# Kernel tuning notes

Measured on AMD Instinct MI355X. Metric: run time of the kernel, lower is better.

Reference implementation:

```python
import jax, jax.numpy as jnp
import numpy as np

N_HEADS = 12


def setup_inputs() -> dict:
    key = jax.random.key(0)
    k1, k2, k3 = jax.random.split(key, 3)
    B, W, C = 2, 2048, 768
    in_sequence_bwc = jax.random.normal(k1, (B, W, C), dtype=jnp.float32)
    # QKV projection weight [3C, C] (torch Linear convention: out_features x in_features)
    w_attn = jax.random.normal(k2, (3 * C, C), dtype=jnp.float32) * (1.0 / np.sqrt(C))
    w_proj = jax.random.normal(k3, (C, C), dtype=jnp.float32) * (1.0 / np.sqrt(C))
    return {"in_sequence_bwc": in_sequence_bwc, "w_attn": w_attn, "w_proj": w_proj}


def reference(in_sequence_bwc, w_attn, w_proj):
    B, W, C = in_sequence_bwc.shape
    H = N_HEADS
    K = C // H  # head dim
    qkv = jnp.einsum('bwc,dc->bwd', in_sequence_bwc, w_attn)  # [B,W,3C]
    q, k, v = jnp.split(qkv, 3, axis=-1)
    # [B,H,W,K]
    q = q.reshape(B, W, H, K).transpose(0, 2, 1, 3)
    k = k.reshape(B, W, H, K).transpose(0, 2, 1, 3)
    v = v.reshape(B, W, H, K).transpose(0, 2, 1, 3)
    scores = jnp.einsum('bhqk,bhsk->bhqs', q, k) / jnp.sqrt(jnp.float32(K))
    causal = jnp.tril(jnp.ones((W, W), dtype=bool))
    scores = jnp.where(causal[None, None], scores, jnp.float32(-jnp.inf))
    probs = jax.nn.softmax(scores, axis=-1)
    out = jnp.einsum('bhqs,bhsk->bhqk', probs, v)  # [B,H,W,K]
    out = out.transpose(0, 2, 1, 3).reshape(B, W, C)
    return jnp.einsum('bwc,dc->bwd', out, w_proj)
```

## Files before the change

kernel.cpp:

```cpp
#include <hip/hip_runtime.h>

constexpr int B_  = 2;
constexpr int W_  = 2048;
constexpr int C_  = 768;
constexpr int H_  = 12;
constexpr int HD  = 64;
constexpr int C3  = 3 * C_;
constexpr int M_  = B_ * W_;
constexpr int NSLOT = 80;

typedef float  f32x4 __attribute__((ext_vector_type(4)));
typedef short  s16x8 __attribute__((ext_vector_type(8)));
typedef short  s16x4 __attribute__((ext_vector_type(4)));
typedef unsigned short u16;
typedef unsigned int   u32;

__device__ __forceinline__ u16 f2bf(float f) {
    unsigned int u = __float_as_uint(f);
    u += 0x7FFFu + ((u >> 16) & 1u);
    return (u16)(u >> 16);
}
__device__ __forceinline__ float bf2f(u16 v) {
    return __uint_as_float(((u32)v) << 16);
}

__device__ __forceinline__ void gload_lds16(const u16* g, u16* l) {
    __builtin_amdgcn_global_load_lds(
        (const __attribute__((address_space(1))) unsigned int*)g,
        (__attribute__((address_space(3))) unsigned int*)l, 16, 0, 0);
}

__global__ __launch_bounds__(256)
void cvt_all(const float* __restrict__ x, const float* __restrict__ wa,
             const float* __restrict__ wp, u16* __restrict__ xb,
             u16* __restrict__ wab, u16* __restrict__ wpb)
{
    const int n0 = M_ * C_ / 8;
    const int n1 = n0 + C3 * C_ / 8;
    const int n2 = n1 + C_ * C_ / 8;
    int i = blockIdx.x * 256 + threadIdx.x;
    const float* s; u16* d; int j;
    if (i < n0)      { s = x;  d = xb;  j = i; }
    else if (i < n1) { s = wa; d = wab; j = i - n0; }
    else if (i < n2) { s = wp; d = wpb; j = i - n1; }
    else return;
    const float4 a = reinterpret_cast<const float4*>(s)[j * 2];
    const float4 b = reinterpret_cast<const float4*>(s)[j * 2 + 1];
    s16x8 v;
    v[0] = (short)f2bf(a.x); v[1] = (short)f2bf(a.y);
    v[2] = (short)f2bf(a.z); v[3] = (short)f2bf(a.w);
    v[4] = (short)f2bf(b.x); v[5] = (short)f2bf(b.y);
    v[6] = (short)f2bf(b.z); v[7] = (short)f2bf(b.w);
    reinterpret_cast<s16x8*>(d)[j] = v;
}

__device__ __forceinline__ void store_out(u16*  p, float v) { *p = f2bf(v); }
__device__ __forceinline__ void store_out(float* p, float v) { *p = v; }

template <typename OutT>
__global__ __launch_bounds__(256)
void gemm_nt_mfma(const u16* __restrict__ A, const u16* __restrict__ Bm,
                  OutT* __restrict__ Y, int Ndim, int Kdim)
{
    __shared__ __align__(16) u16 As[3][128 * 32];
    __shared__ __align__(16) u16 Bs[3][128 * 32];

    const int t  = threadIdx.x;
    const int w  = t >> 6;
    const int l  = t & 63;
    const int lg = l >> 4;
    const int ln = l & 15;
    const int wm = w >> 1;
    const int wn = w & 1;
    const int m0 = blockIdx.x * 128;
    const int n0 = blockIdx.y * 128;

    f32x4 acc[4][4];
    #pragma unroll
    for (int mi = 0; mi < 4; ++mi)
        #pragma unroll
        for (int ni = 0; ni < 4; ++ni)
            acc[mi][ni] = (f32x4){0.f, 0.f, 0.f, 0.f};

    size_t off[2];
    #pragma unroll
    for (int it = 0; it < 2; ++it) {
        const int c  = t + it * 256;
        off[it] = (size_t)((c >> 6) * 16 + (c & 15)) * Kdim + ((c >> 4) & 3) * 8;
    }

    #define GEMM_STAGE(buf, k0s)                                              \
        _Pragma("unroll")                                                     \
        for (int it = 0; it < 2; ++it) {                                      \
            gload_lds16(A  + (size_t)m0 * Kdim + (k0s) + off[it],             \
                        &As[buf][(size_t)(it * 256 + w * 64) * 8]);           \
            gload_lds16(Bm + (size_t)n0 * Kdim + (k0s) + off[it],             \
                        &Bs[buf][(size_t)(it * 256 + w * 64) * 8]);           \
        }

    GEMM_STAGE(0, 0)
    GEMM_STAGE(1, 32)

    int cur = 0;
    for (int k0 = 0; k0 < Kdim; k0 += 32) {
        if (k0 + 32 < Kdim)
            asm volatile("s_waitcnt vmcnt(4)" ::: "memory");
        else
            asm volatile("s_waitcnt vmcnt(0)" ::: "memory");
        __builtin_amdgcn_s_barrier();

        const int nx2 = (cur + 2 >= 3) ? cur - 1 : cur + 2;
        if (k0 + 64 < Kdim) { GEMM_STAGE(nx2, k0 + 64) }

        s16x8 af[4], bf[4];
        #pragma unroll
        for (int mi = 0; mi < 4; ++mi)
            af[mi] = *reinterpret_cast<const s16x8*>(
                &As[cur][(size_t)((wm * 4 + mi) * 64 + l) * 8]);
        #pragma unroll
        for (int ni = 0; ni < 4; ++ni)
            bf[ni] = *reinterpret_cast<const s16x8*>(
                &Bs[cur][(size_t)((wn * 4 + ni) * 64 + l) * 8]);
        #pragma unroll
        for (int mi = 0; mi < 4; ++mi)
            #pragma unroll
            for (int ni = 0; ni < 4; ++ni)
                acc[mi][ni] = __builtin_amdgcn_mfma_f32_16x16x32_bf16(
                    af[mi], bf[ni], acc[mi][ni], 0, 0, 0);

        cur = (cur == 2) ? 0 : cur + 1;
    }
    #undef GEMM_STAGE

    #pragma unroll
    for (int mi = 0; mi < 4; ++mi) {
        const int row = m0 + wm * 64 + mi * 16 + lg * 4;
        #pragma unroll
        for (int ni = 0; ni < 4; ++ni) {
            const int col = n0 + wn * 64 + ni * 16 + ln;
            #pragma unroll
            for (int r = 0; r < 4; ++r)
                store_out(&Y[(size_t)(row + r) * Ndim + col], acc[mi][ni][r]);
        }
    }
}

__global__ __launch_bounds__(256)
void attn_partial(const u16* __restrict__ qkv, u16* __restrict__ po,
                  float* __restrict__ pl)
{
    __shared__ __align__(16) unsigned char KsB[64 * 128];
    __shared__ __align__(16) unsigned char VtB[64 * 144];

    const int t  = threadIdx.x;
    const int w  = t >> 6;
    const int l  = t & 63;
    const int lg = l >> 4;
    const int ln = l & 15;
    const int p  = (NSLOT - 1) - (int)blockIdx.x;
    const int h  = blockIdx.y;
    const int b  = blockIdx.z;

    int qt, ck;
    if (p < 8)       { qt = p;                 ck = 0; }
    else if (p < 24) { qt = 8  + ((p - 8) >> 1);  ck = (p - 8) & 1; }
    else if (p < 48) { qt = 16 + (p - 24) / 3;    ck = (p - 24) % 3; }
    else             { qt = 24 + ((p - 48) >> 2); ck = (p - 48) & 3; }

    const int qb  = qt * 64;
    const int q0w = qb + w * 16;
    const int g0  = ck * 8;
    const int g1  = min(qt + 1, g0 + 8);
    const int slot = (b * H_ + h) * NSLOT + p;

    const u16* base  = qkv + (size_t)(b * W_) * C3;
    const u16* kbase = base + C_ + h * HD;
    const u16* vbase = base + 2 * C_ + h * HD;

    s16x8 qf[2];
    {
        const u16* qrow = base + (size_t)(q0w + ln) * C3 + h * HD;
        #pragma unroll
        for (int kc = 0; kc < 2; ++kc)
            qf[kc] = *reinterpret_cast<const s16x8*>(&qrow[kc * 32 + lg * 8]);
    }

    s16x8 onesf;
    {
        const short v1 = (ln == 0) ? (short)0x3F80 : (short)0;
        #pragma unroll
        for (int i = 0; i < 8; ++i) onesf[i] = v1;
    }

    f32x4 o[4];
    #pragma unroll
    for (int i = 0; i < 4; ++i) o[i] = (f32x4){0.f, 0.f, 0.f, 0.f};
    f32x4 o4 = (f32x4){0.f, 0.f, 0.f, 0.f};

    const float c1 = 0.18033688011112042f;
    const float c2 = 17.312340490667562f;

    const size_t sk_off = (size_t)((t >> 7) * 16 + (t & 15)) * C3
                        + ((t >> 6) & 1) * 32 + ((t >> 4) & 3) * 8;
    const bool vstage = (t < 128);
    const int vrun = (t >> 4) & 7;
    const int vK0  = (vrun >> 2) * 32 + (vrun & 3) * 4;
    const int vdq  = (t & 15) * 4;
    const int kfb  = l * 16;

    s16x8 kr[2];
    s16x4 vr[8];

    {
        const int s0 = g0 * 64;
        const u16* ks = kbase + (size_t)s0 * C3 + sk_off;
        kr[0] = *reinterpret_cast<const s16x8*>(ks);
        kr[1] = *reinterpret_cast<const s16x8*>(ks + (size_t)32 * C3);
        if (vstage) {
            const u16* vsrc = vbase + (size_t)(s0 + vK0) * C3 + vdq;
            #pragma unroll
            for (int e = 0; e < 8; ++e)
                vr[e] = *reinterpret_cast<const s16x4*>(
                    &vsrc[(size_t)((e >> 2) * 16 + (e & 3)) * C3]);
        }
    }

    for (int g = g0; g < g1; ++g) {
        const int s0 = g * 64;

        __syncthreads();

        *reinterpret_cast<s16x8*>(KsB + t * 16)         = kr[0];
        *reinterpret_cast<s16x8*>(KsB + (t + 256) * 16) = kr[1];
        if (vstage) {
            #pragma unroll
            for (int j = 0; j < 4; ++j) {
                s16x8 pk = { vr[0][j], vr[1][j], vr[2][j], vr[3][j],
                             vr[4][j], vr[5][j], vr[6][j], vr[7][j] };
                *reinterpret_cast<s16x8*>(
                    VtB + (vdq + j) * 144 + vrun * 16) = pk;
            }
        }

        if (g + 1 < g1) {
            const int s1 = s0 + 64;
            const u16* ks = kbase + (size_t)s1 * C3 + sk_off;
            kr[0] = *reinterpret_cast<const s16x8*>(ks);
            kr[1] = *reinterpret_cast<const s16x8*>(ks + (size_t)32 * C3);
            if (vstage) {
                const u16* vsrc = vbase + (size_t)(s1 + vK0) * C3 + vdq;
                #pragma unroll
                for (int e = 0; e < 8; ++e)
                    vr[e] = *reinterpret_cast<const s16x4*>(
                        &vsrc[(size_t)((e >> 2) * 16 + (e & 3)) * C3]);
            }
        }

        __syncthreads();

        #pragma unroll
        for (int c = 0; c < 2; ++c) {
            if (s0 + c * 32 <= q0w + 15) {
                float pt[2][4];
                #pragma unroll
                for (int n2 = 0; n2 < 2; ++n2) {
                    const unsigned char* kfrag = KsB + (c * 2 + n2) * 2048 + kfb;
                    s16x8 kf0 = *reinterpret_cast<const s16x8*>(kfrag);
                    s16x8 kf1 = *reinterpret_cast<const s16x8*>(kfrag + 1024);
                    f32x4 s = (f32x4){0.f, 0.f, 0.f, 0.f};
                    __builtin_amdgcn_s_setprio(1);
                    s = __builtin_amdgcn_mfma_f32_16x16x32_bf16(kf0, qf[0], s, 0, 0, 0);
                    s = __builtin_amdgcn_mfma_f32_16x16x32_bf16(kf1, qf[1], s, 0, 0, 0);
                    __builtin_amdgcn_s_setprio(0);
                    const int kg0   = s0 + c * 32 + n2 * 16 + lg * 4;
                    const int klast = s0 + c * 32 + n2 * 16 + 15;
                    if (klast <= q0w) {
                        #pragma unroll
                        for (int r = 0; r < 4; ++r)
                            pt[n2][r] = exp2f(fmaf(s[r], c1, -c2));
                    } else {
                        const int qg = q0w + ln;
                        #pragma unroll
                        for (int r = 0; r < 4; ++r)
                            pt[n2][r] = (kg0 + r <= qg)
                                      ? exp2f(fmaf(s[r], c1, -c2)) : 0.0f;
                    }
                }
                union { s16x8 v; u32 wd[4]; } afu;
                asm("v_cvt_pk_bf16_f32 %0, %1, %2"
                    : "=v"(afu.wd[0]) : "v"(pt[0][0]), "v"(pt[0][1]));
                asm("v_cvt_pk_bf16_f32 %0, %1, %2"
                    : "=v"(afu.wd[1]) : "v"(pt[0][2]), "v"(pt[0][3]));
                asm("v_cvt_pk_bf16_f32 %0, %1, %2"
                    : "=v"(afu.wd[2]) : "v"(pt[1][0]), "v"(pt[1][1]));
                asm("v_cvt_pk_bf16_f32 %0, %1, %2"
                    : "=v"(afu.wd[3]) : "v"(pt[1][2]), "v"(pt[1][3]));
                const s16x8 af = afu.v;
                s16x8 vf[4];
                #pragma unroll
                for (int dt = 0; dt < 4; ++dt)
                    vf[dt] = *reinterpret_cast<const s16x8*>(
                        VtB + (dt * 16 + ln) * 144 + c * 64 + lg * 16);
                __builtin_amdgcn_s_setprio(1);
                #pragma unroll
                for (int dt = 0; dt < 4; ++dt)
                    o[dt] = __builtin_amdgcn_mfma_f32_16x16x32_bf16(af, vf[dt], o[dt], 0, 0, 0);
                o4 = __builtin_amdgcn_mfma_f32_16x16x32_bf16(af, onesf, o4, 0, 0, 0);
                __builtin_amdgcn_s_setprio(0);
            }
        }
    }

    if (ln == 0) {
        #pragma unroll
        for (int r = 0; r < 4; ++r)
            pl[(size_t)slot * 64 + w * 16 + lg * 4 + r] = o4[r];
    }
    u16* os = po + (size_t)slot * 4096;
    #pragma unroll
    for (int r = 0; r < 4; ++r)
        #pragma unroll
        for (int dt = 0; dt < 4; ++dt)
            os[(w * 16 + lg * 4 + r) * 64 + dt * 16 + ln] = f2bf(o[dt][r]);
}

__global__ __launch_bounds__(256)
void attn_combine(const u16* __restrict__ po, const float* __restrict__ pl,
                  u16* __restrict__ aob)
{
    const int qt = blockIdx.x;
    const int h  = blockIdx.y;
    const int b  = blockIdx.z;
    const int nc = (qt + 8) >> 3;
    int cum;
    if (qt < 8)       cum = qt;
    else if (qt < 16) cum = 8  + 2 * (qt - 8);
    else if (qt < 24) cum = 24 + 3 * (qt - 16);
    else              cum = 48 + 4 * (qt - 24);
    const int slot0 = (b * H_ + h) * NSLOT + cum;

    const int tid = threadIdx.x;
    const int i   = tid >> 2;
    const int d0  = (tid & 3) * 16;

    float acc[16] = {};
    float lt = 0.0f;
    for (int c = 0; c < nc; ++c) {
        const u16* os = po + (size_t)(slot0 + c) * 4096 + i * 64 + d0;
        s16x8 v0 = *reinterpret_cast<const s16x8*>(os);
        s16x8 v1 = *reinterpret_cast<const s16x8*>(os + 8);
        #pragma unroll
        for (int e = 0; e < 8; ++e) {
            acc[e]     += bf2f((u16)v0[e]);
            acc[8 + e] += bf2f((u16)v1[e]);
        }
        lt += pl[(size_t)(slot0 + c) * 64 + i];
    }
    const float inv = 1.0f / lt;

    u16* dst = aob + (size_t)(b * W_ + qt * 64 + i) * C_ + h * HD + d0;
    s16x8 ov[2];
    #pragma unroll
    for (int e = 0; e < 8; ++e) {
        ov[0][e] = (short)f2bf(acc[e] * inv);
        ov[1][e] = (short)f2bf(acc[8 + e] * inv);
    }
    *reinterpret_cast<s16x8*>(dst)     = ov[0];
    *reinterpret_cast<s16x8*>(dst + 8) = ov[1];
}

extern "C" void kernel_launch(void* const* d_in, const int* in_sizes, int n_in,
                              void* d_out, int out_size, void* d_ws, size_t ws_size,
                              hipStream_t stream)
{
    const float* x      = (const float*)d_in[0];
    const float* w_attn = (const float*)d_in[1];
    const float* w_proj = (const float*)d_in[2];
    float* out = (float*)d_out;

    u16* xb   = (u16*)d_ws;
    u16* wab  = xb   + (size_t)M_ * C_;
    u16* wpb  = wab  + (size_t)C3 * C_;
    u16* qkvb = wpb  + (size_t)C_ * C_;
    u16* aob  = qkvb + (size_t)M_ * C3;
    u16* po   = aob  + (size_t)M_ * C_;
    float* pl = (float*)(po + (size_t)B_ * H_ * NSLOT * 4096);

    {
        const int total8 = (M_ * C_ + C3 * C_ + C_ * C_) / 8;
        cvt_all<<<(total8 + 255) / 256, 256, 0, stream>>>(
            x, w_attn, w_proj, xb, wab, wpb);
    }

    {
        dim3 grid(M_ / 128, C3 / 128);
        gemm_nt_mfma<u16><<<grid, 256, 0, stream>>>(xb, wab, qkvb, C3, C_);
    }

    {
        dim3 grid(NSLOT, H_, B_);
        attn_partial<<<grid, 256, 0, stream>>>(qkvb, po, pl);
    }
    {
        dim3 grid(W_ / 64, H_, B_);
        attn_combine<<<grid, 256, 0, stream>>>(po, pl, aob);
    }

    {
        dim3 grid(M_ / 128, C_ / 128);
        gemm_nt_mfma<float><<<grid, 256, 0, stream>>>(aob, wpb, out, C_, C_);
    }
}
```

Measured before the change: 117.9 us.

## Double attention query tile to 128 rows per block to reuse K/V tiles

Result: slower. 121.7 us (+3.2%).

```diff
diff --git a/kernel.cpp b/kernel.cpp
--- a/kernel.cpp
+++ b/kernel.cpp
@@ -7,7 +7,7 @@
 constexpr int HD  = 64;
 constexpr int C3  = 3 * C_;
 constexpr int M_  = B_ * W_;
-constexpr int NSLOT = 80;
+constexpr int NSLOT = 40;
 
 typedef float  f32x4 __attribute__((ext_vector_type(4)));
 typedef short  s16x8 __attribute__((ext_vector_type(8)));
@@ -162,27 +162,28 @@
     const int b  = blockIdx.z;
 
     int qt, ck;
-    if (p < 8)       { qt = p;                 ck = 0; }
-    else if (p < 24) { qt = 8  + ((p - 8) >> 1);  ck = (p - 8) & 1; }
-    else if (p < 48) { qt = 16 + (p - 24) / 3;    ck = (p - 24) % 3; }
-    else             { qt = 24 + ((p - 48) >> 2); ck = (p - 48) & 3; }
-
-    const int qb  = qt * 64;
-    const int q0w = qb + w * 16;
+    if (p < 4)       { qt = p;                  ck = 0; }
+    else if (p < 12) { qt = 4  + ((p - 4) >> 1);  ck = (p - 4) & 1; }
+    else if (p < 24) { qt = 8  + (p - 12) / 3;    ck = (p - 12) % 3; }
+    else             { qt = 12 + ((p - 24) >> 2); ck = (p - 24) & 3; }
+
+    const int qb  = qt * 128;
+    const int q0w = qb + w * 32;
     const int g0  = ck * 8;
-    const int g1  = min(qt + 1, g0 + 8);
+    const int g1  = min(2 * (qt + 1), g0 + 8);
     const int slot = (b * H_ + h) * NSLOT + p;
 
     const u16* base  = qkv + (size_t)(b * W_) * C3;
     const u16* kbase = base + C_ + h * HD;
     const u16* vbase = base + 2 * C_ + h * HD;
 
-    s16x8 qf[2];
-    {
-        const u16* qrow = base + (size_t)(q0w + ln) * C3 + h * HD;
+    s16x8 qf[2][2];
+    #pragma unroll
+    for (int m = 0; m < 2; ++m) {
+        const u16* qrow = base + (size_t)(q0w + m * 16 + ln) * C3 + h * HD;
         #pragma unroll
         for (int kc = 0; kc < 2; ++kc)
-            qf[kc] = *reinterpret_cast<const s16x8*>(&qrow[kc * 32 + lg * 8]);
+            qf[m][kc] = *reinterpret_cast<const s16x8*>(&qrow[kc * 32 + lg * 8]);
     }
 
     s16x8 onesf;
@@ -192,10 +193,12 @@
         for (int i = 0; i < 8; ++i) onesf[i] = v1;
     }
 
-    f32x4 o[4];
-    #pragma unroll
-    for (int i = 0; i < 4; ++i) o[i] = (f32x4){0.f, 0.f, 0.f, 0.f};
-    f32x4 o4 = (f32x4){0.f, 0.f, 0.f, 0.f};
+    f32x4 o[2][4];
+    #pragma unroll
+    for (int m = 0; m < 2; ++m)
+        #pragma unroll
+        for (int i = 0; i < 4; ++i) o[m][i] = (f32x4){0.f, 0.f, 0.f, 0.f};
+    f32x4 o4[2] = { (f32x4){0.f,0.f,0.f,0.f}, (f32x4){0.f,0.f,0.f,0.f} };
 
     const float c1 = 0.18033688011112042f;
     const float c2 = 17.312340490667562f;
@@ -260,68 +263,88 @@
 
         #pragma unroll
         for (int c = 0; c < 2; ++c) {
-            if (s0 + c * 32 <= q0w + 15) {
-                float pt[2][4];
+            if (s0 + c * 32 <= q0w + 31) {
+                const bool act0 = (s0 + c * 32 <= q0w + 15);
+                float pt[2][2][4];
                 #pragma unroll
                 for (int n2 = 0; n2 < 2; ++n2) {
                     const unsigned char* kfrag = KsB + (c * 2 + n2) * 2048 + kfb;
                     s16x8 kf0 = *reinterpret_cast<const s16x8*>(kfrag);
                     s16x8 kf1 = *reinterpret_cast<const s16x8*>(kfrag + 1024);
-                    f32x4 s = (f32x4){0.f, 0.f, 0.f, 0.f};
-                    __builtin_amdgcn_s_setprio(1);
-                    s = __builtin_amdgcn_mfma_f32_16x16x32_bf16(kf0, qf[0], s, 0, 0, 0);
-                    s = __builtin_amdgcn_mfma_f32_16x16x32_bf16(kf1, qf[1], s, 0, 0, 0);
-                    __builtin_amdgcn_s_setprio(0);
-                    const int kg0   = s0 + c * 32 + n2 * 16 + lg * 4;
-                    const int klast = s0 + c * 32 + n2 * 16 + 15;
-                    if (klast <= q0w) {
-                        #pragma unroll
-                        for (int r = 0; r < 4; ++r)
-                            pt[n2][r] = exp2f(fmaf(s[r], c1, -c2));
-                    } else {
-                        const int qg = q0w + ln;
-                        #pragma unroll
-                        for (int r = 0; r < 4; ++r)
-                            pt[n2][r] = (kg0 + r <= qg)
-                                      ? exp2f(fmaf(s[r], c1, -c2)) : 0.0f;
+                    #pragma unroll
+                    for (int m = 0; m < 2; ++m) {
+                        if (m == 1 || act0) {
+                            f32x4 s = (f32x4){0.f, 0.f, 0.f, 0.f};
+                            __builtin_amdgcn_s_setprio(1);
+                            s = __builtin_amdgcn_mfma_f32_16x16x32_bf16(
+                                kf0, qf[m][0], s, 0, 0, 0);
+                            s = __builtin_amdgcn_mfma_f32_16x16x32_bf16(
+                                kf1, qf[m][1], s, 0, 0, 0);
+                            __builtin_amdgcn_s_setprio(0);
+                            const int kg0   = s0 + c * 32 + n2 * 16 + lg * 4;
+                            const int klast = s0 + c * 32 + n2 * 16 + 15;
+                            const int qbase = q0w + m * 16;
+                            if (klast <= qbase) {
+                                #pragma unroll
+                                for (int r = 0; r < 4; ++r)
+                                    pt[m][n2][r] = exp2f(fmaf(s[r], c1, -c2));
+                            } else {
+                                const int qg = qbase + ln;
+                                #pragma unroll
+                                for (int r = 0; r < 4; ++r)
+                                    pt[m][n2][r] = (kg0 + r <= qg)
+                                              ? exp2f(fmaf(s[r], c1, -c2)) : 0.0f;
+                            }
+                        }
                     }
                 }
-                union { s16x8 v; u32 wd[4]; } afu;
-                asm("v_cvt_pk_bf16_f32 %0, %1, %2"
-                    : "=v"(afu.wd[0]) : "v"(pt[0][0]), "v"(pt[0][1]));
-                asm("v_cvt_pk_bf16_f32 %0, %1, %2"
-                    : "=v"(afu.wd[1]) : "v"(pt[0][2]), "v"(pt[0][3]));
-                asm("v_cvt_pk_bf16_f32 %0, %1, %2"
-                    : "=v"(afu.wd[2]) : "v"(pt[1][0]), "v"(pt[1][1]));
-                asm("v_cvt_pk_bf16_f32 %0, %1, %2"
-                    : "=v"(afu.wd[3]) : "v"(pt[1][2]), "v"(pt[1][3]));
-                const s16x8 af = afu.v;
                 s16x8 vf[4];
                 #pragma unroll
                 for (int dt = 0; dt < 4; ++dt)
                     vf[dt] = *reinterpret_cast<const s16x8*>(
                         VtB + (dt * 16 + ln) * 144 + c * 64 + lg * 16);
-                __builtin_amdgcn_s_setprio(1);
                 #pragma unroll
-                for (int dt = 0; dt < 4; ++dt)
-                    o[dt] = __builtin_amdgcn_mfma_f32_16x16x32_bf16(af, vf[dt], o[dt], 0, 0, 0);
-                o4 = __builtin_amdgcn_mfma_f32_16x16x32_bf16(af, onesf, o4, 0, 0, 0);
-                __builtin_amdgcn_s_setprio(0);
+                for (int m = 0; m < 2; ++m) {
+                    if (m == 1 || act0) {
+                        union { s16x8 v; u32 wd[4]; } afu;
+                        asm("v_cvt_pk_bf16_f32 %0, %1, %2"
+                            : "=v"(afu.wd[0]) : "v"(pt[m][0][0]), "v"(pt[m][0][1]));
+                        asm("v_cvt_pk_bf16_f32 %0, %1, %2"
+                            : "=v"(afu.wd[1]) : "v"(pt[m][0][2]), "v"(pt[m][0][3]));
+                        asm("v_cvt_pk_bf16_f32 %0, %1, %2"
+                            : "=v"(afu.wd[2]) : "v"(pt[m][1][0]), "v"(pt[m][1][1]));
+                        asm("v_cvt_pk_bf16_f32 %0, %1, %2"
+                            : "=v"(afu.wd[3]) : "v"(pt[m][1][2]), "v"(pt[m][1][3]));
+                        const s16x8 af = afu.v;
+                        __builtin_amdgcn_s_setprio(1);
+                        #pragma unroll
+                        for (int dt = 0; dt < 4; ++dt)
+                            o[m][dt] = __builtin_amdgcn_mfma_f32_16x16x32_bf16(
+                                af, vf[dt], o[m][dt], 0, 0, 0);
+                        o4[m] = __builtin_amdgcn_mfma_f32_16x16x32_bf16(
+                            af, onesf, o4[m], 0, 0, 0);
+                        __builtin_amdgcn_s_setprio(0);
+                    }
+                }
             }
         }
     }
 
-    if (ln == 0) {
+    #pragma unroll
+    for (int m = 0; m < 2; ++m) {
+        if (ln == 0) {
+            #pragma unroll
+            for (int r = 0; r < 4; ++r)
+                pl[(size_t)slot * 128 + w * 32 + m * 16 + lg * 4 + r] = o4[m][r];
+        }
+        u16* os = po + (size_t)slot * 8192;
         #pragma unroll
         for (int r = 0; r < 4; ++r)
-            pl[(size_t)slot * 64 + w * 16 + lg * 4 + r] = o4[r];
-    }
-    u16* os = po + (size_t)slot * 4096;
-    #pragma unroll
-    for (int r = 0; r < 4; ++r)
-        #pragma unroll
-        for (int dt = 0; dt < 4; ++dt)
-            os[(w * 16 + lg * 4 + r) * 64 + dt * 16 + ln] = f2bf(o[dt][r]);
+            #pragma unroll
+            for (int dt = 0; dt < 4; ++dt)
+                os[(w * 32 + m * 16 + lg * 4 + r) * 64 + dt * 16 + ln] =
+                    f2bf(o[m][dt][r]);
+    }
 }
 
 __global__ __launch_bounds__(256)
@@ -331,42 +354,40 @@
     const int qt = blockIdx.x;
     const int h  = blockIdx.y;
     const int b  = blockIdx.z;
-    const int nc = (qt + 8) >> 3;
+    const int nc = (qt + 4) >> 2;
     int cum;
-    if (qt < 8)       cum = qt;
-    else if (qt < 16) cum = 8  + 2 * (qt - 8);
-    else if (qt < 24) cum = 24 + 3 * (qt - 16);
-    else              cum = 48 + 4 * (qt - 24);
+    if (qt < 4)       cum = qt;
+    else if (qt < 8)  cum = 4  + 2 * (qt - 4);
+    else if (qt < 12) cum = 12 + 3 * (qt - 8);
+    else              cum = 24 + 4 * (qt - 12);
     const int slot0 = (b * H_ + h) * NSLOT + cum;
 
     const int tid = threadIdx.x;
-    const int i   = tid >> 2;
-    const int d0  = (tid & 3) * 16;
-
-    float acc[16] = {};
+    const int i   = tid >> 1;
+    const int d0  = (tid & 1) * 32;
+
+    float acc[32] = {};
     float lt = 0.0f;
     for (int c = 0; c < nc; ++c) {
-        const u16* os = po + (size_t)(slot0 + c) * 4096 + i * 64 + d0;
-        s16x8 v0 = *reinterpret_cast<const s16x8*>(os);
-        s16x8 v1 = *reinterpret_cast<const s16x8*>(os + 8);
-        #pragma unroll
-        for (int e = 0; e < 8; ++e) {
-            acc[e]     += bf2f((u16)v0[e]);
-            acc[8 + e] += bf2f((u16)v1[e]);
-        }
-        lt += pl[(size_t)(slot0 + c) * 64 + i];
+        const u16* os = po + (size_t)(slot0 + c) * 8192 + i * 64 + d0;
+        #pragma unroll
+        for (int v = 0; v < 4; ++v) {
+            s16x8 vv = *reinterpret_cast<const s16x8*>(os + v * 8);
+            #pragma unroll
+            for (int e = 0; e < 8; ++e) acc[v * 8 + e] += bf2f((u16)vv[e]);
+        }
+        lt += pl[(size_t)(slot0 + c) * 128 + i];
     }
     const float inv = 1.0f / lt;
 
-    u16* dst = aob + (size_t)(b * W_ + qt * 64 + i) * C_ + h * HD + d0;
-    s16x8 ov[2];
-    #pragma unroll
-    for (int e = 0; e < 8; ++e) {
-        ov[0][e] = (short)f2bf(acc[e] * inv);
-        ov[1][e] = (short)f2bf(acc[8 + e] * inv);
-    }
-    *reinterpret_cast<s16x8*>(dst)     = ov[0];
-    *reinterpret_cast<s16x8*>(dst + 8) = ov[1];
+    u16* dst = aob + (size_t)(b * W_ + qt * 128 + i) * C_ + h * HD + d0;
+    #pragma unroll
+    for (int v = 0; v < 4; ++v) {
+        s16x8 ov;
+        #pragma unroll
+        for (int e = 0; e < 8; ++e) ov[e] = (short)f2bf(acc[v * 8 + e] * inv);
+        *reinterpret_cast<s16x8*>(dst + v * 8) = ov;
+    }
 }
 
 extern "C" void kernel_launch(void* const* d_in, const int* in_sizes, int n_in,
@@ -384,7 +405,7 @@
     u16* qkvb = wpb  + (size_t)C_ * C_;
     u16* aob  = qkvb + (size_t)M_ * C3;
     u16* po   = aob  + (size_t)M_ * C_;
-    float* pl = (float*)(po + (size_t)B_ * H_ * NSLOT * 4096);
+    float* pl = (float*)(po + (size_t)B_ * H_ * NSLOT * 8192);
 
     {
         const int total8 = (M_ * C_ + C3 * C_ + C_ * C_) / 8;
@@ -402,7 +423,7 @@
         attn_partial<<<grid, 256, 0, stream>>>(qkvb, po, pl);
     }
     {
-        dim3 grid(W_ / 64, H_, B_);
+        dim3 grid(W_ / 128, H_, B_);
         attn_combine<<<grid, 256, 0, stream>>>(po, pl, aob);
     }
 
```
